# Optimization experiments

Measured on AMD Instinct MI355X. Metric: run time of the kernel, lower is better.

## Reference

```python
import jax, jax.numpy as jnp
import numpy as np

EPS = 1e-12


def agnn_layer(x, row, col, num_nodes):
    """AGNN propagation with beta frozen at 1.0 (requires_grad=False in source).
    alpha_ij = softmax_{j in N(i)} ( beta * cos(x_i, x_j) ); out_i = sum_j alpha_ij * x_j.
    row = destination node of each edge (segment id), col = source node.
    """
    xn = x / (jnp.linalg.norm(x, axis=-1, keepdims=True) + EPS)  # unit-norm features
    score = jnp.sum(xn[row] * xn[col], axis=-1)                   # [E] beta=1 * cos sim
    smax = jax.ops.segment_max(score, row, num_segments=num_nodes)
    e = jnp.exp(score - smax[row])                                # stable softmax numerator
    denom = jax.ops.segment_sum(e, row, num_segments=num_nodes)
    alpha = e / jnp.maximum(denom[row], EPS)                      # [E]
    out = jax.ops.segment_sum(alpha[:, None] * x[col], row, num_segments=num_nodes)
    return out


def setup_inputs() -> dict:
    key = jax.random.key(0)
    ks = jax.random.split(key, 8)
    N, E = 100000, 1600000
    IN_DIM, HID, OUT_DIM = 128, 64, 64
    x = jax.random.normal(ks[0], (N, IN_DIM), dtype=jnp.float32)
    edge_row = jnp.sort(jax.random.randint(ks[1], (E,), 0, N))
    edge_col = jax.random.randint(ks[2], (E,), 0, N)
    # Linear params (PyTorch nn.Linear style: y = x @ W.T + b)
    s1 = 1.0 / np.sqrt(IN_DIM)
    W1 = jax.random.uniform(ks[3], (HID, IN_DIM), jnp.float32, -s1, s1)
    b1 = jax.random.uniform(ks[4], (HID,), jnp.float32, -s1, s1)
    s2 = 1.0 / np.sqrt(HID)
    W2 = jax.random.uniform(ks[5], (OUT_DIM, HID), jnp.float32, -s2, s2)
    b2 = jax.random.uniform(ks[6], (OUT_DIM,), jnp.float32, -s2, s2)
    return {"x": x, "edge_row": edge_row, "edge_col": edge_col,
            "W1": W1, "b1": b1, "W2": W2, "b2": b2}


def reference(x, edge_row, edge_col, W1, b1, W2, b2):
    N = x.shape[0]
    h = jax.nn.relu(x @ W1.T + b1)
    for _ in range(4):  # 4 frozen-beta AGNN layers
        h = jax.nn.relu(agnn_layer(h, edge_row, edge_col, N))
    return h @ W2.T + b2
```

## Files before the change

kernel.cpp:

```cpp
#include <hip/hip_runtime.h>


typedef _Float16 h2 __attribute__((ext_vector_type(2)));

union U4H { uint4 u; h2 h[4]; };
union U2H { uint2 u; h2 h[2]; };
union UHI { unsigned u; h2 h; };

#define DEV_INLINE __device__ __forceinline__

DEV_INLINE h2 mkh2(float a, float b) {
    h2 r; r.x = (_Float16)a; r.y = (_Float16)b; return r;
}

__global__ __launch_bounds__(256) void build_rowptr_scan(const int* __restrict__ row,
                                                         int* __restrict__ ptr,
                                                         int N, int E) {
    int e = blockIdx.x * blockDim.x + threadIdx.x;
    if (e >= E) return;
    const int r1 = row[e];
    const int r0 = (e == 0) ? -1 : row[e - 1];
    for (int i = r0 + 1; i <= r1; ++i) ptr[i] = e;
    if (e == E - 1) {
        for (int i = r1 + 1; i <= N; ++i) ptr[i] = E;
    }
}

#define PSEG 1024
__global__ __launch_bounds__(1024) void build_perm_seg(const int* __restrict__ ptr,
                                                       int* __restrict__ perm,
                                                       int N) {
    __shared__ int hist[256];
    __shared__ int tmp[256];
    const int t    = threadIdx.x;
    const int base = blockIdx.x * PSEG;
    const int end  = (base + PSEG < N) ? base + PSEG : N;
    const int cnt  = end - base;

    if (t < 256) hist[t] = 0;
    __syncthreads();

    int d = -1;
    if (t < cnt) {
        d = ptr[base + t + 1] - ptr[base + t];
        if (d > 255) d = 255;
        atomicAdd(&hist[d], 1);
    }
    __syncthreads();

    int h0 = (t < 256) ? hist[t] : 0;
    int* src = hist; int* dst = tmp;
    for (int off = 1; off < 256; off <<= 1) {
        if (t < 256) dst[t] = src[t] + (t >= off ? src[t - off] : 0);
        __syncthreads();
        int* tt = src; src = dst; dst = tt;
    }
    if (t < 256) src[t] -= h0;
    __syncthreads();

    if (t < cnt) {
        int pos = base + atomicAdd(&src[d], 1);
        perm[pos] = base + t;
    }
}

__global__ __launch_bounds__(512) void gemm1_relu(const float* __restrict__ x,
                                                  const float* __restrict__ W1,
                                                  const float* __restrict__ b1,
                                                  unsigned short* __restrict__ xn,
                                                  float* __restrict__ nrm,
                                                  int N) {
    __shared__ __align__(16) float Wt[32 * 64];
    __shared__ __align__(16) float xT[32 * 128];
    const int tid  = threadIdx.x;
    const int tx   = tid & 15;
    const int ty   = tid >> 4;
    const int base = blockIdx.x * 128;

    const float4* W4  = (const float4*)W1;
    const float4* x4p = (const float4*)x;

    const int wO  = tid & 63;
    const int wK4 = tid >> 6;
    const int mA  = tid & 127;
    const int kA  = tid >> 7;
    const int mB  = mA;
    const int kB  = kA + 4;
    const int nodeA = base + mA;

    float4 wv, xa_, xb_;
    wv = W4[wO * 32 + wK4];
    xa_ = make_float4(0.f, 0.f, 0.f, 0.f);
    xb_ = xa_;
    if (nodeA < N) {
        xa_ = x4p[(size_t)nodeA * 32 + kA];
        xb_ = x4p[(size_t)nodeA * 32 + kB];
    }

    float4 b4 = ((const float4*)b1)[tx];
    float4 acc[4];
    acc[0] = b4; acc[1] = b4; acc[2] = b4; acc[3] = b4;

    for (int c = 0; c < 4; ++c) {
        Wt[(4 * wK4 + 0) * 64 + wO] = wv.x;
        Wt[(4 * wK4 + 1) * 64 + wO] = wv.y;
        Wt[(4 * wK4 + 2) * 64 + wO] = wv.z;
        Wt[(4 * wK4 + 3) * 64 + wO] = wv.w;
        xT[(4 * kA + 0) * 128 + mA] = xa_.x;
        xT[(4 * kA + 1) * 128 + mA] = xa_.y;
        xT[(4 * kA + 2) * 128 + mA] = xa_.z;
        xT[(4 * kA + 3) * 128 + mA] = xa_.w;
        xT[(4 * kB + 0) * 128 + mB] = xb_.x;
        xT[(4 * kB + 1) * 128 + mB] = xb_.y;
        xT[(4 * kB + 2) * 128 + mB] = xb_.z;
        xT[(4 * kB + 3) * 128 + mB] = xb_.w;
        __syncthreads();

        if (c < 3) {
            const int ko = (c + 1) * 8;
            wv = W4[wO * 32 + ko + wK4];
            if (nodeA < N) {
                xa_ = x4p[(size_t)nodeA * 32 + ko + kA];
                xb_ = x4p[(size_t)nodeA * 32 + ko + kB];
            }
        }

#pragma unroll 4
        for (int k = 0; k < 32; ++k) {
            const float4 w4 = *(const float4*)&Wt[k * 64 + 4 * tx];
            const float4 xv = *(const float4*)&xT[k * 128 + 4 * ty];
            acc[0].x = fmaf(xv.x, w4.x, acc[0].x);
            acc[0].y = fmaf(xv.x, w4.y, acc[0].y);
            acc[0].z = fmaf(xv.x, w4.z, acc[0].z);
            acc[0].w = fmaf(xv.x, w4.w, acc[0].w);
            acc[1].x = fmaf(xv.y, w4.x, acc[1].x);
            acc[1].y = fmaf(xv.y, w4.y, acc[1].y);
            acc[1].z = fmaf(xv.y, w4.z, acc[1].z);
            acc[1].w = fmaf(xv.y, w4.w, acc[1].w);
            acc[2].x = fmaf(xv.z, w4.x, acc[2].x);
            acc[2].y = fmaf(xv.z, w4.y, acc[2].y);
            acc[2].z = fmaf(xv.z, w4.z, acc[2].z);
            acc[2].w = fmaf(xv.z, w4.w, acc[2].w);
            acc[3].x = fmaf(xv.w, w4.x, acc[3].x);
            acc[3].y = fmaf(xv.w, w4.y, acc[3].y);
            acc[3].z = fmaf(xv.w, w4.z, acc[3].z);
            acc[3].w = fmaf(xv.w, w4.w, acc[3].w);
        }
        if (c < 3) __syncthreads();
    }

#pragma unroll
    for (int mm = 0; mm < 4; ++mm) {
        float4 r = acc[mm];
        r.x = fmaxf(r.x, 0.f); r.y = fmaxf(r.y, 0.f);
        r.z = fmaxf(r.z, 0.f); r.w = fmaxf(r.w, 0.f);
        float s = fmaf(r.x, r.x, fmaf(r.y, r.y, fmaf(r.z, r.z, r.w * r.w)));
        s += __shfl_xor(s, 1, 64);
        s += __shfl_xor(s, 2, 64);
        s += __shfl_xor(s, 4, 64);
        s += __shfl_xor(s, 8, 64);
        const float nn  = sqrtf(s) + 1e-12f;
        const float inv = 1.f / nn;
        int node = base + 4 * ty + mm;
        if (node < N) {
            U2H pk;
            pk.h[0] = mkh2(r.x * inv, r.y * inv);
            pk.h[1] = mkh2(r.z * inv, r.w * inv);
            *(uint2*)&xn[(size_t)node * 64 + 4 * tx] = pk.u;
            if (tx == mm) nrm[node] = nn;
        }
    }
}

__global__ __launch_bounds__(256) void agnn_layer(const uint4* __restrict__ xn4,
                                                  const float* __restrict__ nrm,
                                                  const int* __restrict__ ptr,
                                                  const int* __restrict__ col,
                                                  const int* __restrict__ perm,
                                                  uint4* __restrict__ xo4,
                                                  float* __restrict__ nrmo,
                                                  int N) {
    const int tid  = threadIdx.x;
    const int lane = tid & 63;
    const int g    = (lane >> 3) & 1;
    const int sub  = lane & 7;
    const int slot = blockIdx.x * 16 + (tid >> 4);
    if (slot >= N) return;
    const int i = perm[slot];

    U4H hi_;
    hi_.u = xn4[(unsigned)i * 8u + sub];
    {
        const _Float16 L2E = (_Float16)1.4426950408889634f;
        h2 l2 = {L2E, L2E};
#pragma unroll
        for (int t = 0; t < 4; ++t) hi_.h[t] *= l2;
    }

    const int p0  = ptr[i], p1 = ptr[i + 1];
    const int mid = p0 + ((p1 - p0 + 1) >> 1);
    int       t   = g ? mid : p0;
    const int e_  = g ? p1  : mid;

    float den = 0.f;
    U4H acc;
    acc.h[0] = mkh2(0.f, 0.f); acc.h[1] = mkh2(0.f, 0.f);
    acc.h[2] = mkh2(0.f, 0.f); acc.h[3] = mkh2(0.f, 0.f);

#define EDGE_BODY(VU, NRMJ)                                                  \
    {                                                                        \
        U4H xa; xa.u = (VU);                                                 \
        float s = 0.f;                                                       \
        s = __builtin_amdgcn_fdot2(hi_.h[0], xa.h[0], s, false);             \
        s = __builtin_amdgcn_fdot2(hi_.h[1], xa.h[1], s, false);             \
        s = __builtin_amdgcn_fdot2(hi_.h[2], xa.h[2], s, false);             \
        s = __builtin_amdgcn_fdot2(hi_.h[3], xa.h[3], s, false);             \
        s += __shfl_xor(s, 1, 64);                                           \
        s += __shfl_xor(s, 2, 64);                                           \
        s += __shfl_xor(s, 4, 64);                                           \
        const float p = exp2f(s);                                            \
        den += p;                                                            \
        const _Float16 wh = (_Float16)(p * (NRMJ));                          \
        h2 w2 = {wh, wh};                                                    \
        acc.h[0] += w2 * xa.h[0];                                            \
        acc.h[1] += w2 * xa.h[1];                                            \
        acc.h[2] += w2 * xa.h[2];                                            \
        acc.h[3] += w2 * xa.h[3];                                            \
    }

    {
        const int n_ = e_ - t;
        int j0 = 0, j1 = 0, j2 = 0, j3 = 0;
        uint4 v0 = make_uint4(0u, 0u, 0u, 0u), v1 = v0;
        float n0 = 0.f, n1 = 0.f;
        if (n_ > 0) j0 = col[t];
        if (n_ > 1) j1 = col[t + 1];
        if (n_ > 0) { v0 = xn4[(unsigned)j0 * 8u + sub]; n0 = nrm[j0]; }
        if (n_ > 1) { v1 = xn4[(unsigned)j1 * 8u + sub]; n1 = nrm[j1]; }
        if (n_ > 2) j2 = col[t + 2];
        if (n_ > 3) j3 = col[t + 3];

        while (t + 5 < e_) {
            const uint4 v2 = xn4[(unsigned)j2 * 8u + sub];
            const float m2 = nrm[j2];
            const uint4 v3 = xn4[(unsigned)j3 * 8u + sub];
            const float m3 = nrm[j3];
            const int j4 = col[t + 4];
            const int j5 = col[t + 5];
            EDGE_BODY(v0, n0)
            EDGE_BODY(v1, n1)
            v0 = v2; n0 = m2; v1 = v3; n1 = m3;
            j2 = j4; j3 = j5;
            t += 2;
        }
        const int rem = e_ - t;
        if (rem > 2) {
            const uint4 v2 = xn4[(unsigned)j2 * 8u + sub];
            const float m2 = nrm[j2];
            uint4 v3 = make_uint4(0u, 0u, 0u, 0u);
            float m3 = 0.f;
            if (rem > 3) { v3 = xn4[(unsigned)j3 * 8u + sub]; m3 = nrm[j3]; }
            int j4 = 0;
            if (rem > 4) j4 = col[t + 4];
            EDGE_BODY(v0, n0)
            EDGE_BODY(v1, n1)
            EDGE_BODY(v2, m2)
            if (rem > 3) EDGE_BODY(v3, m3)
            if (rem > 4) {
                const uint4 v4 = xn4[(unsigned)j4 * 8u + sub];
                const float m4 = nrm[j4];
                EDGE_BODY(v4, m4)
            }
        } else {
            if (rem > 0) EDGE_BODY(v0, n0)
            if (rem > 1) EDGE_BODY(v1, n1)
        }
    }
#undef EDGE_BODY

    {
        den += __shfl_xor(den, 8, 64);
#pragma unroll
        for (int t2 = 0; t2 < 4; ++t2) {
            UHI a; a.h = acc.h[t2];
            UHI b; b.u = (unsigned)__shfl_xor((int)a.u, 8, 64);
            acc.h[t2] = a.h + b.h;
        }
    }

    const float id = 1.f / fmaxf(den, 1e-12f);
    float o[8];
#pragma unroll
    for (int t2 = 0; t2 < 4; ++t2) {
        o[2 * t2]     = fmaxf((float)acc.h[t2].x * id, 0.f);
        o[2 * t2 + 1] = fmaxf((float)acc.h[t2].y * id, 0.f);
    }

    float s2 = 0.f;
#pragma unroll
    for (int t2 = 0; t2 < 8; ++t2) s2 = fmaf(o[t2], o[t2], s2);
    s2 += __shfl_xor(s2, 1, 64);
    s2 += __shfl_xor(s2, 2, 64);
    s2 += __shfl_xor(s2, 4, 64);
    const float nn  = sqrtf(s2) + 1e-12f;
    const float inv = 1.f / nn;

    if (g == 0) {
        U4H ov;
        ov.h[0] = mkh2(o[0] * inv, o[1] * inv);
        ov.h[1] = mkh2(o[2] * inv, o[3] * inv);
        ov.h[2] = mkh2(o[4] * inv, o[5] * inv);
        ov.h[3] = mkh2(o[6] * inv, o[7] * inv);
        xo4[(unsigned)i * 8u + sub] = ov.u;
        if (sub == 0) nrmo[i] = nn;
    }
}

__global__ __launch_bounds__(512) void gemm2(const unsigned short* __restrict__ xn,
                                             const float* __restrict__ nrm,
                                             const float* __restrict__ W2,
                                             const float* __restrict__ b2,
                                             float* __restrict__ out,
                                             int N) {
    __shared__ __align__(16) float Wt[64 * 64];
    __shared__ __align__(16) float xT[64 * 128];
    const int tid  = threadIdx.x;
    const int tx   = tid & 15;
    const int ty   = tid >> 4;
    const int base = blockIdx.x * 128;

    {
        const float4* W4 = (const float4*)W2;
#pragma unroll
        for (int it = 0; it < 2; ++it) {
            int idx = tid + it * 512;
            int o = idx & 63, k4 = idx >> 6;
            float4 v = W4[o * 16 + k4];
            Wt[(4 * k4 + 0) * 64 + o] = v.x;
            Wt[(4 * k4 + 1) * 64 + o] = v.y;
            Wt[(4 * k4 + 2) * 64 + o] = v.z;
            Wt[(4 * k4 + 3) * 64 + o] = v.w;
        }
        const uint2* x2 = (const uint2*)xn;
#pragma unroll
        for (int it = 0; it < 4; ++it) {
            int idx = tid + it * 512;
            int mm = idx & 127, k4 = idx >> 7;
            int node = base + mm;
            U2H v; v.u = make_uint2(0u, 0u);
            float nn = 0.f;
            if (node < N) { v.u = x2[(size_t)node * 16 + k4]; nn = nrm[node]; }
            xT[(4 * k4 + 0) * 128 + mm] = (float)v.h[0].x * nn;
            xT[(4 * k4 + 1) * 128 + mm] = (float)v.h[0].y * nn;
            xT[(4 * k4 + 2) * 128 + mm] = (float)v.h[1].x * nn;
            xT[(4 * k4 + 3) * 128 + mm] = (float)v.h[1].y * nn;
        }
    }
    __syncthreads();

    float4 b4 = ((const float4*)b2)[tx];
    float4 acc[4];
    acc[0] = b4; acc[1] = b4; acc[2] = b4; acc[3] = b4;

#pragma unroll 4
    for (int k = 0; k < 64; ++k) {
        const float4 w4 = *(const float4*)&Wt[k * 64 + 4 * tx];
        const float4 xv = *(const float4*)&xT[k * 128 + 4 * ty];
        acc[0].x = fmaf(xv.x, w4.x, acc[0].x);
        acc[0].y = fmaf(xv.x, w4.y, acc[0].y);
        acc[0].z = fmaf(xv.x, w4.z, acc[0].z);
        acc[0].w = fmaf(xv.x, w4.w, acc[0].w);
        acc[1].x = fmaf(xv.y, w4.x, acc[1].x);
        acc[1].y = fmaf(xv.y, w4.y, acc[1].y);
        acc[1].z = fmaf(xv.y, w4.z, acc[1].z);
        acc[1].w = fmaf(xv.y, w4.w, acc[1].w);
        acc[2].x = fmaf(xv.z, w4.x, acc[2].x);
        acc[2].y = fmaf(xv.z, w4.y, acc[2].y);
        acc[2].z = fmaf(xv.z, w4.z, acc[2].z);
        acc[2].w = fmaf(xv.z, w4.w, acc[2].w);
        acc[3].x = fmaf(xv.w, w4.x, acc[3].x);
        acc[3].y = fmaf(xv.w, w4.y, acc[3].y);
        acc[3].z = fmaf(xv.w, w4.z, acc[3].z);
        acc[3].w = fmaf(xv.w, w4.w, acc[3].w);
    }

#pragma unroll
    for (int mm = 0; mm < 4; ++mm) {
        int node = base + 4 * ty + mm;
        if (node < N) *(float4*)&out[(size_t)node * 64 + 4 * tx] = acc[mm];
    }
}

extern "C" void kernel_launch(void* const* d_in, const int* in_sizes, int n_in,
                              void* d_out, int out_size, void* d_ws, size_t ws_size,
                              hipStream_t stream) {
    const float* x   = (const float*)d_in[0];
    const int*   row = (const int*)d_in[1];
    const int*   col = (const int*)d_in[2];
    const float* W1  = (const float*)d_in[3];
    const float* b1  = (const float*)d_in[4];
    const float* W2  = (const float*)d_in[5];
    const float* b2  = (const float*)d_in[6];
    float* out = (float*)d_out;

    const int N = in_sizes[0] / 128;
    const int E = in_sizes[1];

    char* ws = (char*)d_ws;
    size_t off = 0;
    unsigned short* ha = (unsigned short*)(ws + off); off += (size_t)N * 64 * 2;
    unsigned short* hb = (unsigned short*)(ws + off); off += (size_t)N * 64 * 2;
    float* na_  = (float*)(ws + off); off += (size_t)N * sizeof(float);
    float* nb_  = (float*)(ws + off); off += (size_t)N * sizeof(float);
    int*   ptr  = (int*)  (ws + off); off += (size_t)(N + 1) * sizeof(int);
    off = (off + 15) & ~(size_t)15;
    int*   perm = (int*)  (ws + off); off += (size_t)N * sizeof(int);
    (void)ws_size; (void)n_in; (void)out_size;

    build_rowptr_scan<<<(E + 255) / 256, 256, 0, stream>>>(row, ptr, N, E);

    build_perm_seg<<<(N + PSEG - 1) / PSEG, 1024, 0, stream>>>(ptr, perm, N);

    const int nbG = (N + 127) / 128;
    gemm1_relu<<<nbG, 512, 0, stream>>>(x, W1, b1, ha, na_, N);

    const int nb16 = (N + 15) / 16;
    unsigned short* hc = ha; unsigned short* hn = hb;
    float* nc = na_; float* nn = nb_;
    for (int l = 0; l < 4; ++l) {
        agnn_layer<<<nb16, 256, 0, stream>>>((const uint4*)hc, nc, ptr, col, perm,
                                             (uint4*)hn, nn, N);
        unsigned short* t = hc; hc = hn; hn = t;
        float* tf = nc; nc = nn; nn = tf;
    }

    gemm2<<<nbG, 512, 0, stream>>>(hc, nc, W2, b2, out, N);
}
```

Baseline: 300.4 us.

## Persistent grid-stride AGNN layer with prefetched node metadata and DPP reductions

The AGNN layer kernel becomes persistent: a fixed grid of 2048 blocks strides over degree-sorted node slots, prefetching the next node's metadata and self-feature row while finishing the current one. The permutation array becomes an int4 record holding node id, row start and row end, so the kernel no longer reads perm and then ptr through a dependent chain. Cross-lane reductions switch from __shfl_xor to DPP row operations, and the dot product is split into two accumulators to shorten the dependency chain. The risks are some load imbalance from the fixed grid and higher register pressure under the new occupancy hint.

```diff
diff --git a/kernel.cpp b/kernel.cpp
--- a/kernel.cpp
+++ b/kernel.cpp
@@ -6,11 +6,20 @@
 union U4H { uint4 u; h2 h[4]; };
 union U2H { uint2 u; h2 h[2]; };
 union UHI { unsigned u; h2 h; };
+union UF  { unsigned u; float f; int i; };
 
 #define DEV_INLINE __device__ __forceinline__
 
 DEV_INLINE h2 mkh2(float a, float b) {
     h2 r; r.x = (_Float16)a; r.y = (_Float16)b; return r;
+}
+
+template <int CTRL>
+DEV_INLINE float dpp_addf(float x) {
+    UF a, b;
+    a.f = x;
+    b.i = __builtin_amdgcn_update_dpp(0, a.i, CTRL, 0xF, 0xF, true);
+    return x + b.f;
 }
 
 __global__ __launch_bounds__(256) void build_rowptr_scan(const int* __restrict__ row,
@@ -28,7 +37,7 @@
 
 #define PSEG 1024
 __global__ __launch_bounds__(1024) void build_perm_seg(const int* __restrict__ ptr,
-                                                       int* __restrict__ perm,
+                                                       int4* __restrict__ meta,
                                                        int N) {
     __shared__ int hist[256];
     __shared__ int tmp[256];
@@ -40,9 +49,11 @@
     if (t < 256) hist[t] = 0;
     __syncthreads();
 
-    int d = -1;
+    int d = -1, p0v = 0, p1v = 0;
     if (t < cnt) {
-        d = ptr[base + t + 1] - ptr[base + t];
+        p0v = ptr[base + t];
+        p1v = ptr[base + t + 1];
+        d = p1v - p0v;
         if (d > 255) d = 255;
         atomicAdd(&hist[d], 1);
     }
@@ -60,7 +71,7 @@
 
     if (t < cnt) {
         int pos = base + atomicAdd(&src[d], 1);
-        perm[pos] = base + t;
+        meta[pos] = make_int4(base + t, p0v, p1v, 0);
     }
 }
 
@@ -155,10 +166,10 @@
         r.x = fmaxf(r.x, 0.f); r.y = fmaxf(r.y, 0.f);
         r.z = fmaxf(r.z, 0.f); r.w = fmaxf(r.w, 0.f);
         float s = fmaf(r.x, r.x, fmaf(r.y, r.y, fmaf(r.z, r.z, r.w * r.w)));
-        s += __shfl_xor(s, 1, 64);
-        s += __shfl_xor(s, 2, 64);
-        s += __shfl_xor(s, 4, 64);
-        s += __shfl_xor(s, 8, 64);
+        s = dpp_addf<0xB1>(s);
+        s = dpp_addf<0x4E>(s);
+        s = dpp_addf<0x141>(s);
+        s = dpp_addf<0x140>(s);
         const float nn  = sqrtf(s) + 1e-12f;
         const float inv = 1.f / nn;
         int node = base + 4 * ty + mm;
@@ -172,52 +183,60 @@
     }
 }
 
-__global__ __launch_bounds__(256) void agnn_layer(const uint4* __restrict__ xn4,
-                                                  const float* __restrict__ nrm,
-                                                  const int* __restrict__ ptr,
-                                                  const int* __restrict__ col,
-                                                  const int* __restrict__ perm,
-                                                  uint4* __restrict__ xo4,
-                                                  float* __restrict__ nrmo,
-                                                  int N) {
+__global__ __launch_bounds__(256, 8) void agnn_layer(const uint4* __restrict__ xn4,
+                                                     const float* __restrict__ nrm,
+                                                     const int4* __restrict__ meta,
+                                                     const int* __restrict__ col,
+                                                     uint4* __restrict__ xo4,
+                                                     float* __restrict__ nrmo,
+                                                     int N, int stride) {
     const int tid  = threadIdx.x;
     const int lane = tid & 63;
     const int g    = (lane >> 3) & 1;
     const int sub  = lane & 7;
-    const int slot = blockIdx.x * 16 + (tid >> 4);
+    int slot = blockIdx.x * 16 + (tid >> 4);
     if (slot >= N) return;
-    const int i = perm[slot];
-
-    U4H hi_;
-    hi_.u = xn4[(unsigned)i * 8u + sub];
-    {
-        const _Float16 L2E = (_Float16)1.4426950408889634f;
-        h2 l2 = {L2E, L2E};
-#pragma unroll
-        for (int t = 0; t < 4; ++t) hi_.h[t] *= l2;
-    }
-
-    const int p0  = ptr[i], p1 = ptr[i + 1];
-    const int mid = p0 + ((p1 - p0 + 1) >> 1);
-    int       t   = g ? mid : p0;
-    const int e_  = g ? p1  : mid;
-
-    float den = 0.f;
-    U4H acc;
-    acc.h[0] = mkh2(0.f, 0.f); acc.h[1] = mkh2(0.f, 0.f);
-    acc.h[2] = mkh2(0.f, 0.f); acc.h[3] = mkh2(0.f, 0.f);
+
+    int4 m0 = meta[slot];
+    uint4 hraw = xn4[(unsigned)m0.x * 8u + sub];
+
+    for (;;) {
+        const int snext = slot + stride;
+        const int msl   = (snext < N) ? snext : slot;
+        const int4 m1   = meta[msl];
+
+        const int i  = m0.x;
+        const int p0 = m0.y, p1 = m0.z;
+
+        U4H hi_;
+        hi_.u = hraw;
+        {
+            const _Float16 L2E = (_Float16)1.4426950408889634f;
+            h2 l2 = {L2E, L2E};
+#pragma unroll
+            for (int c = 0; c < 4; ++c) hi_.h[c] *= l2;
+        }
+
+        const int mid = p0 + ((p1 - p0 + 1) >> 1);
+        int       t   = g ? mid : p0;
+        const int e_  = g ? p1  : mid;
+
+        float den = 0.f;
+        U4H acc;
+        acc.h[0] = mkh2(0.f, 0.f); acc.h[1] = mkh2(0.f, 0.f);
+        acc.h[2] = mkh2(0.f, 0.f); acc.h[3] = mkh2(0.f, 0.f);
 
 #define EDGE_BODY(VU, NRMJ)                                                  \
     {                                                                        \
         U4H xa; xa.u = (VU);                                                 \
-        float s = 0.f;                                                       \
-        s = __builtin_amdgcn_fdot2(hi_.h[0], xa.h[0], s, false);             \
-        s = __builtin_amdgcn_fdot2(hi_.h[1], xa.h[1], s, false);             \
-        s = __builtin_amdgcn_fdot2(hi_.h[2], xa.h[2], s, false);             \
-        s = __builtin_amdgcn_fdot2(hi_.h[3], xa.h[3], s, false);             \
-        s += __shfl_xor(s, 1, 64);                                           \
-        s += __shfl_xor(s, 2, 64);                                           \
-        s += __shfl_xor(s, 4, 64);                                           \
+        float sa = __builtin_amdgcn_fdot2(hi_.h[0], xa.h[0], 0.f, false);    \
+        sa = __builtin_amdgcn_fdot2(hi_.h[1], xa.h[1], sa, false);           \
+        float sb = __builtin_amdgcn_fdot2(hi_.h[2], xa.h[2], 0.f, false);    \
+        sb = __builtin_amdgcn_fdot2(hi_.h[3], xa.h[3], sb, false);           \
+        float s = sa + sb;                                                   \
+        s = dpp_addf<0xB1>(s);                                               \
+        s = dpp_addf<0x4E>(s);                                               \
+        s = dpp_addf<0x141>(s);                                              \
         const float p = exp2f(s);                                            \
         den += p;                                                            \
         const _Float16 wh = (_Float16)(p * (NRMJ));                          \
@@ -228,91 +247,96 @@
         acc.h[3] += w2 * xa.h[3];                                            \
     }
 
-    {
-        const int n_ = e_ - t;
-        int j0 = 0, j1 = 0, j2 = 0, j3 = 0;
-        uint4 v0 = make_uint4(0u, 0u, 0u, 0u), v1 = v0;
-        float n0 = 0.f, n1 = 0.f;
-        if (n_ > 0) j0 = col[t];
-        if (n_ > 1) j1 = col[t + 1];
-        if (n_ > 0) { v0 = xn4[(unsigned)j0 * 8u + sub]; n0 = nrm[j0]; }
-        if (n_ > 1) { v1 = xn4[(unsigned)j1 * 8u + sub]; n1 = nrm[j1]; }
-        if (n_ > 2) j2 = col[t + 2];
-        if (n_ > 3) j3 = col[t + 3];
-
-        while (t + 5 < e_) {
-            const uint4 v2 = xn4[(unsigned)j2 * 8u + sub];
-            const float m2 = nrm[j2];
-            const uint4 v3 = xn4[(unsigned)j3 * 8u + sub];
-            const float m3 = nrm[j3];
-            const int j4 = col[t + 4];
-            const int j5 = col[t + 5];
-            EDGE_BODY(v0, n0)
-            EDGE_BODY(v1, n1)
-            v0 = v2; n0 = m2; v1 = v3; n1 = m3;
-            j2 = j4; j3 = j5;
-            t += 2;
-        }
-        const int rem = e_ - t;
-        if (rem > 2) {
-            const uint4 v2 = xn4[(unsigned)j2 * 8u + sub];
-            const float m2 = nrm[j2];
-            uint4 v3 = make_uint4(0u, 0u, 0u, 0u);
-            float m3 = 0.f;
-            if (rem > 3) { v3 = xn4[(unsigned)j3 * 8u + sub]; m3 = nrm[j3]; }
-            int j4 = 0;
-            if (rem > 4) j4 = col[t + 4];
-            EDGE_BODY(v0, n0)
-            EDGE_BODY(v1, n1)
-            EDGE_BODY(v2, m2)
-            if (rem > 3) EDGE_BODY(v3, m3)
-            if (rem > 4) {
-                const uint4 v4 = xn4[(unsigned)j4 * 8u + sub];
-                const float m4 = nrm[j4];
-                EDGE_BODY(v4, m4)
+        {
+            const int n_ = e_ - t;
+            int j0 = 0, j1 = 0, j2 = 0, j3 = 0;
+            uint4 v0 = make_uint4(0u, 0u, 0u, 0u), v1 = v0;
+            float n0 = 0.f, n1 = 0.f;
+            if (n_ > 0) j0 = col[t];
+            if (n_ > 1) j1 = col[t + 1];
+            if (n_ > 0) { v0 = xn4[(unsigned)j0 * 8u + sub]; n0 = nrm[j0]; }
+            if (n_ > 1) { v1 = xn4[(unsigned)j1 * 8u + sub]; n1 = nrm[j1]; }
+            if (n_ > 2) j2 = col[t + 2];
+            if (n_ > 3) j3 = col[t + 3];
+
+            while (t + 5 < e_) {
+                const uint4 v2 = xn4[(unsigned)j2 * 8u + sub];
+                const float m2 = nrm[j2];
+                const uint4 v3 = xn4[(unsigned)j3 * 8u + sub];
+                const float m3 = nrm[j3];
+                const int j4 = col[t + 4];
+                const int j5 = col[t + 5];
+                EDGE_BODY(v0, n0)
+                EDGE_BODY(v1, n1)
+                v0 = v2; n0 = m2; v1 = v3; n1 = m3;
+                j2 = j4; j3 = j5;
+                t += 2;
             }
-        } else {
-            if (rem > 0) EDGE_BODY(v0, n0)
-            if (rem > 1) EDGE_BODY(v1, n1)
-        }
-    }
+            const int rem = e_ - t;
+            if (rem > 2) {
+                const uint4 v2 = xn4[(unsigned)j2 * 8u + sub];
+                const float m2 = nrm[j2];
+                uint4 v3 = make_uint4(0u, 0u, 0u, 0u);
+                float m3 = 0.f;
+                if (rem > 3) { v3 = xn4[(unsigned)j3 * 8u + sub]; m3 = nrm[j3]; }
+                int j4 = 0;
+                if (rem > 4) j4 = col[t + 4];
+                EDGE_BODY(v0, n0)
+                EDGE_BODY(v1, n1)
+                EDGE_BODY(v2, m2)
+                if (rem > 3) EDGE_BODY(v3, m3)
+                if (rem > 4) {
+                    const uint4 v4 = xn4[(unsigned)j4 * 8u + sub];
+                    const float m4 = nrm[j4];
+                    EDGE_BODY(v4, m4)
+                }
+            } else {
+                if (rem > 0) EDGE_BODY(v0, n0)
+                if (rem > 1) EDGE_BODY(v1, n1)
+            }
+        }
 #undef EDGE_BODY
 
-    {
-        den += __shfl_xor(den, 8, 64);
-#pragma unroll
-        for (int t2 = 0; t2 < 4; ++t2) {
-            UHI a; a.h = acc.h[t2];
+        hraw = xn4[(unsigned)m1.x * 8u + sub];
+
+        den = dpp_addf<0x140>(den);
+#pragma unroll
+        for (int c = 0; c < 4; ++c) {
+            UHI a; a.h = acc.h[c];
             UHI b; b.u = (unsigned)__shfl_xor((int)a.u, 8, 64);
-            acc.h[t2] = a.h + b.h;
-        }
-    }
-
-    const float id = 1.f / fmaxf(den, 1e-12f);
-    float o[8];
-#pragma unroll
-    for (int t2 = 0; t2 < 4; ++t2) {
-        o[2 * t2]     = fmaxf((float)acc.h[t2].x * id, 0.f);
-        o[2 * t2 + 1] = fmaxf((float)acc.h[t2].y * id, 0.f);
-    }
-
-    float s2 = 0.f;
-#pragma unroll
-    for (int t2 = 0; t2 < 8; ++t2) s2 = fmaf(o[t2], o[t2], s2);
-    s2 += __shfl_xor(s2, 1, 64);
-    s2 += __shfl_xor(s2, 2, 64);
-    s2 += __shfl_xor(s2, 4, 64);
-    const float nn  = sqrtf(s2) + 1e-12f;
-    const float inv = 1.f / nn;
-
-    if (g == 0) {
-        U4H ov;
-        ov.h[0] = mkh2(o[0] * inv, o[1] * inv);
-        ov.h[1] = mkh2(o[2] * inv, o[3] * inv);
-        ov.h[2] = mkh2(o[4] * inv, o[5] * inv);
-        ov.h[3] = mkh2(o[6] * inv, o[7] * inv);
-        xo4[(unsigned)i * 8u + sub] = ov.u;
-        if (sub == 0) nrmo[i] = nn;
+            acc.h[c] = a.h + b.h;
+        }
+
+        const float id = 1.f / fmaxf(den, 1e-12f);
+        float o[8];
+#pragma unroll
+        for (int c = 0; c < 4; ++c) {
+            o[2 * c]     = fmaxf((float)acc.h[c].x * id, 0.f);
+            o[2 * c + 1] = fmaxf((float)acc.h[c].y * id, 0.f);
+        }
+
+        float s2 = 0.f;
+#pragma unroll
+        for (int c = 0; c < 8; ++c) s2 = fmaf(o[c], o[c], s2);
+        s2 = dpp_addf<0xB1>(s2);
+        s2 = dpp_addf<0x4E>(s2);
+        s2 = dpp_addf<0x141>(s2);
+        const float nn  = sqrtf(s2) + 1e-12f;
+        const float inv = 1.f / nn;
+
+        if (g == 0) {
+            U4H ov;
+            ov.h[0] = mkh2(o[0] * inv, o[1] * inv);
+            ov.h[1] = mkh2(o[2] * inv, o[3] * inv);
+            ov.h[2] = mkh2(o[4] * inv, o[5] * inv);
+            ov.h[3] = mkh2(o[6] * inv, o[7] * inv);
+            xo4[(unsigned)i * 8u + sub] = ov.u;
+            if (sub == 0) nrmo[i] = nn;
+        }
+
+        if (snext >= N) break;
+        slot = snext;
+        m0 = m1;
     }
 }
 
@@ -414,22 +438,26 @@
     float* nb_  = (float*)(ws + off); off += (size_t)N * sizeof(float);
     int*   ptr  = (int*)  (ws + off); off += (size_t)(N + 1) * sizeof(int);
     off = (off + 15) & ~(size_t)15;
-    int*   perm = (int*)  (ws + off); off += (size_t)N * sizeof(int);
+    int4*  meta = (int4*) (ws + off); off += (size_t)N * sizeof(int4);
     (void)ws_size; (void)n_in; (void)out_size;
 
     build_rowptr_scan<<<(E + 255) / 256, 256, 0, stream>>>(row, ptr, N, E);
 
-    build_perm_seg<<<(N + PSEG - 1) / PSEG, 1024, 0, stream>>>(ptr, perm, N);
+    build_perm_seg<<<(N + PSEG - 1) / PSEG, 1024, 0, stream>>>(ptr, meta, N);
 
     const int nbG = (N + 127) / 128;
     gemm1_relu<<<nbG, 512, 0, stream>>>(x, W1, b1, ha, na_, N);
 
-    const int nb16 = (N + 15) / 16;
+    int nbA = 2048;
+    const int maxB = (N + 15) / 16;
+    if (nbA > maxB) nbA = maxB;
+    const int stride = nbA * 16;
+
     unsigned short* hc = ha; unsigned short* hn = hb;
     float* nc = na_; float* nn = nb_;
     for (int l = 0; l < 4; ++l) {
-        agnn_layer<<<nb16, 256, 0, stream>>>((const uint4*)hc, nc, ptr, col, perm,
-                                             (uint4*)hn, nn, N);
+        agnn_layer<<<nbA, 256, 0, stream>>>((const uint4*)hc, nc, meta, col,
+                                            (uint4*)hn, nn, N, stride);
         unsigned short* t = hc; hc = hn; hn = t;
         float* tf = nc; nc = nn; nn = tf;
     }
```

Result: slower. 329.8 us (+9.8%).
